# Kernel tuning notes

Hardware: AMD Instinct MI355X
Metric: run time of the kernel (lower is better)

The kernel has to match this reference:

```python
import math
import jax, jax.numpy as jnp
import numpy as np

BS, C, HH, HW = 32, 64, 128, 128   # x is NCHW; C == dim
S0, S1 = 2, 2                      # patch size
DIM = 64
K = 512                            # num_embeddings


def setup_inputs() -> dict:
    key = jax.random.key(0)
    k1, k2 = jax.random.split(key)
    x = jax.random.normal(k1, (BS, C, HH, HW), dtype=jnp.float32)
    embed = jax.random.normal(k2, (S0, S1, DIM, K), dtype=jnp.float32) * 0.02
    return {"x": x, "embed": embed}


def reference(x, embed):
    # eval-mode forward (not training): sample = one_hot(argmax(probs))
    bs, Cc, hH, hW = x.shape
    rH, rW = hH // S0, hW // S1
    xp = jnp.transpose(x, (0, 2, 3, 1))                          # [b, hH, hW, C]
    xb = xp.reshape(bs, rH, S0, rW, S1, Cc)
    xb = jnp.transpose(xb, (0, 1, 3, 2, 4, 5))                   # [b, rH, rW, s0, s1, C]
    flat = xb.reshape(-1, S0 * S1 * Cc)                          # [T, D]
    E = embed.reshape(-1, K)                                     # [D, K]
    # squared-distance via matmul
    distances = (jnp.sum(flat * flat, axis=1, keepdims=True)
                 - 2.0 * (flat @ E)
                 + jnp.sum(E * E, axis=0, keepdims=True))        # [T, K]
    logits = jax.nn.log_softmax(-distances, axis=-1)             # dist.logits (normalized)
    probs = jnp.exp(logits)                                      # dist.probs
    embed_ind_flat = jnp.argmax(probs, axis=-1)                  # [T]
    sample = jax.nn.one_hot(embed_ind_flat, K, dtype=flat.dtype) # [T, K]
    embed_ind = embed_ind_flat.reshape(bs, rH, rW)
    quantize = jnp.einsum('tk,hwdk->thwd', sample, embed)        # [T, s0, s1, dim]
    quantize = quantize.reshape(bs, rH, rW, S0, S1, Cc)
    quantize = jnp.transpose(quantize, (0, 1, 3, 2, 4, 5)).reshape(bs, hH, hW, Cc)
    quantize = jnp.transpose(quantize, (0, 3, 1, 2))             # [b, C, hH, hW]
    KL = jnp.where(probs == 0, 0.0, probs * (logits + math.log(K)))
    diff = KL.sum() / bs * (32 * 32 * 3.0)
    diff = diff * 0.0
    avg_probs = jnp.mean(sample, axis=1)                         # [T] (faithful: mean over K)
    perplexity = jnp.exp(-jnp.sum(avg_probs * jnp.log(avg_probs + 1e-10), axis=-1))
    return quantize, diff, embed_ind, perplexity
```

## Files before the change

### kernel.cpp

```cpp
#include <hip/hip_runtime.h>


#define OFF_DIFF    33554432
#define OFF_IND     33554433
#define OFF_PERP    33685505

typedef __attribute__((ext_vector_type(8))) short short8;
typedef __attribute__((ext_vector_type(4))) float f32x4;

__device__ __forceinline__ unsigned short f2bf(float f) {
    unsigned int u = __float_as_uint(f);
    return (unsigned short)((u + 0x7FFFu + ((u >> 16) & 1u)) >> 16);
}
__device__ __forceinline__ float bf2f(unsigned short h) {
    return __uint_as_float(((unsigned int)h) << 16);
}

__device__ __forceinline__ void gload_lds16(const void* g, void* l) {
    __builtin_amdgcn_global_load_lds(
        (const __attribute__((address_space(1))) unsigned int*)g,
        (__attribute__((address_space(3))) unsigned int*)l, 16, 0, 0);
}

__global__ void vq_split(const float* __restrict__ E,
                         float* __restrict__ Et,
                         short* __restrict__ EhiSw,
                         short* __restrict__ EloSw,
                         float* __restrict__ ssqe,
                         float* __restrict__ out) {
    const int k = blockIdx.x;
    const int t = threadIdx.x;
    float v[4];
    #pragma unroll
    for (int j = 0; j < 4; ++j) v[j] = E[(t * 4 + j) * 512 + k];
    *(float4*)&Et[k * 256 + t * 4] = make_float4(v[0], v[1], v[2], v[3]);

    unsigned short h[4], l[4];
    #pragma unroll
    for (int j = 0; j < 4; ++j) {
        h[j] = f2bf(v[j]);
        l[j] = f2bf(v[j] - bf2f(h[j]));
    }
    uint2 H = make_uint2((unsigned)h[0] | ((unsigned)h[1] << 16),
                         (unsigned)h[2] | ((unsigned)h[3] << 16));
    uint2 L = make_uint2((unsigned)l[0] | ((unsigned)l[1] << 16),
                         (unsigned)l[2] | ((unsigned)l[3] << 16));
    int pos = k * 256 + 8 * ((t >> 1) ^ (k & 7)) + (t & 1) * 4;
    *(uint2*)&EhiSw[pos] = H;
    *(uint2*)&EloSw[pos] = L;

    float s = fmaf(v[0], v[0], fmaf(v[1], v[1], fmaf(v[2], v[2], v[3] * v[3])));
    #pragma unroll
    for (int m = 1; m < 64; m <<= 1) s += __shfl_xor(s, m, 64);
    if (t == 0) {
        ssqe[k] = s;
        if (k == 0) {
            out[OFF_DIFF] = 0.0f;
            out[OFF_PERP] = 0.0f;
        }
    }
}

__device__ __forceinline__ void stage4(short* Th, short* Tl, int lt, int f,
                                       int dbase,
                                       float a, float b, float c, float d) {
    int idx = lt * 256 + (dbase ^ (f << 3));
    unsigned short h0 = f2bf(a), h1 = f2bf(b), h2 = f2bf(c), h3 = f2bf(d);
    *(uint2*)&Th[idx] = make_uint2((unsigned)h0 | ((unsigned)h1 << 16),
                                   (unsigned)h2 | ((unsigned)h3 << 16));
    unsigned short l0 = f2bf(a - bf2f(h0)), l1 = f2bf(b - bf2f(h1));
    unsigned short l2 = f2bf(c - bf2f(h2)), l3 = f2bf(d - bf2f(h3));
    *(uint2*)&Tl[idx] = make_uint2((unsigned)l0 | ((unsigned)l1 << 16),
                                   (unsigned)l2 | ((unsigned)l3 << 16));
}

#define MFMA(A, B, C) __builtin_amdgcn_mfma_f32_16x16x32_bf16(A, B, C, 0, 0, 0)
#define FSWZ(lt) ((((lt) >> 1) ^ ((lt) >> 4)) & 7)

__global__ __launch_bounds__(256, 4)
void vq_main_mfma(const float* __restrict__ x,
                  const float* __restrict__ Et,
                  const short* __restrict__ EhiSw,
                  const short* __restrict__ EloSw,
                  const float* __restrict__ ssqe,
                  float* __restrict__ out) {
    __shared__ __attribute__((aligned(16))) unsigned char smem[35328];
    short* Thi = (short*)smem;
    short* Tlo = (short*)(smem + 16384);
    float* Q   = (float*)smem;
    float* ssqe_sh = (float*)(smem + 33024);
    int*   kstar   = (int*)(smem + 35072);

    const int g   = blockIdx.x;
    const int b   = g >> 6;
    const int rh  = g & 63;
    const int tid = threadIdx.x;
    const int wv  = tid >> 6;
    const int ln  = tid & 63;
    const int r   = ln & 15;
    const int tq  = ln >> 4;
    const int tokr = wv * 16 + r;

    ssqe_sh[tid]       = ssqe[tid];
    ssqe_sh[tid + 256] = ssqe[tid + 256];

    short8 Bh[8], Bl[8];
    const float* xrow = x + (size_t)b * 1048576 + (size_t)rh * 256;

    #pragma unroll
    for (int hp = 0; hp < 2; ++hp) {
        #pragma unroll
        for (int i = 0; i < 2; ++i) {
            int j     = tid + i * 256;
            int col4h = j & 15;
            int rest  = j >> 4;
            int c4    = rest & 15;
            int s0    = rest >> 4;
            const float* p = xrow + (c4 * 4) * 16384 + s0 * 128 + hp * 64 + col4h * 4;
            float4 v0 = *(const float4*)(p);
            float4 v1 = *(const float4*)(p + 16384);
            float4 v2 = *(const float4*)(p + 32768);
            float4 v3 = *(const float4*)(p + 49152);
            int ltA = col4h * 2, ltB = ltA + 1;
            int fA = FSWZ(ltA), fB = FSWZ(ltB);
            int d0 = s0 * 128 + c4 * 4, d1 = d0 + 64;
            stage4(Thi, Tlo, ltA, fA, d0, v0.x, v1.x, v2.x, v3.x);
            stage4(Thi, Tlo, ltA, fA, d1, v0.y, v1.y, v2.y, v3.y);
            stage4(Thi, Tlo, ltB, fB, d0, v0.z, v1.z, v2.z, v3.z);
            stage4(Thi, Tlo, ltB, fB, d1, v0.w, v1.w, v2.w, v3.w);
        }
        __syncthreads();
        if ((tokr >> 5) == hp) {
            int lt = tokr & 31;
            int f  = FSWZ(lt);
            #pragma unroll
            for (int ks = 0; ks < 8; ++ks) {
                int idx = lt * 256 + ((ks * 32 + tq * 8) ^ (f << 3));
                Bh[ks] = *(const short8*)&Thi[idx];
                Bl[ks] = *(const short8*)&Tlo[idx];
            }
        }
        __syncthreads();
    }

    {
        const char* hs = (const char*)EhiSw;
        const char* ls = (const char*)EloSw;
        char* d = (char*)smem;
        int o = wv * 1024 + ln * 16;
        gload_lds16(hs + o,        d + wv * 1024);
        gload_lds16(hs + o + 4096, d + wv * 1024 + 4096);
        gload_lds16(ls + o,        d + wv * 1024 + 8192);
        gload_lds16(ls + o + 4096, d + wv * 1024 + 12288);
    }
    __syncthreads();

    float best  = __builtin_inff();
    int   besti = 0;
    int   cur   = 0;

    for (int ct = 0; ct < 32; ++ct) {
        if (ct < 31) {
            const char* hs = (const char*)EhiSw + (ct + 1) * 8192;
            const char* ls = (const char*)EloSw + (ct + 1) * 8192;
            char* d = (char*)smem + (cur ^ 1) * 16384;
            int o = wv * 1024 + ln * 16;
            gload_lds16(hs + o,        d + wv * 1024);
            gload_lds16(hs + o + 4096, d + wv * 1024 + 4096);
            gload_lds16(ls + o,        d + wv * 1024 + 8192);
            gload_lds16(ls + o + 4096, d + wv * 1024 + 12288);
        }
        const short* bh = (const short*)(smem + cur * 16384);
        const short* bl = bh + 4096;
        f32x4 ae = {0.f, 0.f, 0.f, 0.f};
        f32x4 ao = {0.f, 0.f, 0.f, 0.f};
        #pragma unroll
        for (int ks = 0; ks < 8; ks += 2) {
            int off0 = r * 256 + 8 * ((ks * 4 + tq) ^ (r & 7));
            short8 ah0 = *(const short8*)&bh[off0];
            short8 al0 = *(const short8*)&bl[off0];
            int off1 = r * 256 + 8 * (((ks + 1) * 4 + tq) ^ (r & 7));
            short8 ah1 = *(const short8*)&bh[off1];
            short8 al1 = *(const short8*)&bl[off1];
            ae = MFMA(ah0, Bh[ks], ae);
            ao = MFMA(ah1, Bh[ks + 1], ao);
            ae = MFMA(ah0, Bl[ks], ae);
            ao = MFMA(ah1, Bl[ks + 1], ao);
            ae = MFMA(al0, Bh[ks], ae);
            ao = MFMA(al1, Bh[ks + 1], ao);
        }
        float4 sq = *(const float4*)&ssqe_sh[ct * 16 + tq * 4];
        int kb = ct * 16 + tq * 4;
        float s0v = fmaf(-2.0f, ae[0] + ao[0], sq.x);
        float s1v = fmaf(-2.0f, ae[1] + ao[1], sq.y);
        float s2v = fmaf(-2.0f, ae[2] + ao[2], sq.z);
        float s3v = fmaf(-2.0f, ae[3] + ao[3], sq.w);
        if (s0v < best) { best = s0v; besti = kb;     }
        if (s1v < best) { best = s1v; besti = kb + 1; }
        if (s2v < best) { best = s2v; besti = kb + 2; }
        if (s3v < best) { best = s3v; besti = kb + 3; }
        __syncthreads();
        cur ^= 1;
    }

    #pragma unroll
    for (int m = 16; m <= 32; m <<= 1) {
        float ob = __shfl_xor(best, m, 64);
        int   oi = __shfl_xor(besti, m, 64);
        if (ob < best || (ob == best && oi < besti)) { best = ob; besti = oi; }
    }
    if (tq == 0) {
        kstar[tokr] = besti;
        out[OFF_IND + (size_t)g * 64 + tokr] = (float)besti;
    }
    __syncthreads();

    #pragma unroll
    for (int hp = 0; hp < 2; ++hp) {
        if (hp) __syncthreads();
        {
            int qt = tid & 31, part = tid >> 5;
            const float* Erow = Et + (size_t)kstar[hp * 32 + qt] * 256 + part * 32;
            float* qrow = Q + qt * 257 + part * 32;
            #pragma unroll
            for (int u = 0; u < 8; ++u) {
                float4 vv = *(const float4*)(Erow + u * 4);
                qrow[u * 4]     = vv.x;
                qrow[u * 4 + 1] = vv.y;
                qrow[u * 4 + 2] = vv.z;
                qrow[u * 4 + 3] = vv.w;
            }
        }
        __syncthreads();
        float* ob2 = out + (size_t)b * 1048576 + rh * 256 + hp * 64;
        #pragma unroll
        for (int i = 0; i < 8; ++i) {
            int j     = tid + i * 256;
            int col4h = j & 15;
            int rest  = j >> 4;
            int c  = rest >> 1;
            int s0 = rest & 1;
            int ltA = col4h * 2, ltB = ltA + 1;
            int d0 = s0 * 128 + c, d1 = d0 + 64;
            float4 v;
            v.x = Q[ltA * 257 + d0];
            v.y = Q[ltA * 257 + d1];
            v.z = Q[ltB * 257 + d0];
            v.w = Q[ltB * 257 + d1];
            *(float4*)(ob2 + c * 16384 + s0 * 128 + col4h * 4) = v;
        }
    }
}

__global__ void vq_prep(const float* __restrict__ E,
                        float* __restrict__ ssqe,
                        float* __restrict__ out) {
    int k = blockIdx.x * 256 + threadIdx.x;
    float acc = 0.0f;
    #pragma unroll 8
    for (int d = 0; d < 256; ++d) {
        float e = E[d * 512 + k];
        acc = fmaf(e, e, acc);
    }
    ssqe[k] = acc;
    if (k == 0) { out[OFF_DIFF] = 0.0f; out[OFF_PERP] = 0.0f; }
}

__global__ __launch_bounds__(256, 2)
void vq_main_f32(const float* __restrict__ x,
                 const float* __restrict__ E,
                 const float* __restrict__ ssqe,
                 float* __restrict__ out) {
    __shared__ float A[256 * 64];
    __shared__ float redD[4][64];
    __shared__ int   redI[4][64];
    __shared__ int   kstar_sh[64];

    const int g = blockIdx.x, b = g >> 6, rh = g & 63, tid = threadIdx.x;
    const float* xbase = x + (size_t)b * 1048576 + rh * 256;

    #pragma unroll
    for (int i = 0; i < 16; ++i) {
        int j = tid + i * 256;
        int row = j >> 5, col4 = j & 31;
        int c = row >> 1, s0 = row & 1;
        const float4 v = *(const float4*)(xbase + c * 16384 + s0 * 128 + col4 * 4);
        int tokk = col4 * 2;
        int d0 = s0 * 128 + c, d1 = d0 + 64;
        *(float2*)&A[d0 * 64 + tokk] = make_float2(v.x, v.z);
        *(float2*)&A[d1 * 64 + tokk] = make_float2(v.y, v.w);
    }
    __syncthreads();

    const int wave = tid >> 6, lane = tid & 63;
    float ssq = 0.0f;
    #pragma unroll 8
    for (int d = 0; d < 256; ++d) { float a = A[d * 64 + lane]; ssq = fmaf(a, a, ssq); }

    const int K0 = __builtin_amdgcn_readfirstlane(wave * 128);
    float best = __builtin_inff();
    int besti = 0;
    for (int chunk = 0; chunk < 8; ++chunk) {
        const int k0 = K0 + chunk * 16;
        const float* __restrict__ Ep = E + k0;
        float acc[16];
        #pragma unroll
        for (int j = 0; j < 16; ++j) acc[j] = 0.0f;
        #pragma unroll 4
        for (int d = 0; d < 256; ++d) {
            float a = A[d * 64 + lane];
            #pragma unroll
            for (int j = 0; j < 16; ++j) acc[j] = fmaf(a, Ep[d * 512 + j], acc[j]);
        }
        #pragma unroll
        for (int j = 0; j < 16; ++j) {
            float dist = (ssq - 2.0f * acc[j]) + ssqe[k0 + j];
            if (dist < best) { best = dist; besti = k0 + j; }
        }
    }
    redD[wave][lane] = best; redI[wave][lane] = besti;
    __syncthreads();
    if (tid < 64) {
        float bd = redD[0][tid]; int bi = redI[0][tid];
        #pragma unroll
        for (int w = 1; w < 4; ++w) {
            float dd = redD[w][tid];
            if (dd < bd) { bd = dd; bi = redI[w][tid]; }
        }
        kstar_sh[tid] = bi;
        out[OFF_IND + g * 64 + tid] = (float)bi;
    }
    __syncthreads();
    float* obase = out + (size_t)b * 1048576 + rh * 256;
    #pragma unroll
    for (int i = 0; i < 16; ++i) {
        int j = tid + i * 256;
        int row = j >> 5, col4 = j & 31;
        int c = row >> 1, s0 = row & 1;
        int tokA = col4 * 2, tokB = tokA + 1;
        int kA = kstar_sh[tokA], kB = kstar_sh[tokB];
        int d0 = s0 * 128 + c, d1 = d0 + 64;
        float4 v;
        v.x = E[d0 * 512 + kA]; v.y = E[d1 * 512 + kA];
        v.z = E[d0 * 512 + kB]; v.w = E[d1 * 512 + kB];
        *(float4*)(obase + c * 16384 + s0 * 128 + col4 * 4) = v;
    }
}

extern "C" void kernel_launch(void* const* d_in, const int* in_sizes, int n_in,
                              void* d_out, int out_size, void* d_ws, size_t ws_size,
                              hipStream_t stream) {
    const float* x = (const float*)d_in[0];
    const float* E = (const float*)d_in[1];
    float* out = (float*)d_out;

    float* ssqe  = (float*)d_ws;
    float* Et    = (float*)((char*)d_ws + 4096);
    short* EhiSw = (short*)((char*)d_ws + 528384);
    short* EloSw = (short*)((char*)d_ws + 790528);
    const size_t need = 1052672;

    if (ws_size >= need) {
        hipLaunchKernelGGL(vq_split, dim3(512), dim3(64), 0, stream,
                           E, Et, EhiSw, EloSw, ssqe, out);
        hipLaunchKernelGGL(vq_main_mfma, dim3(2048), dim3(256), 0, stream,
                           x, Et, EhiSw, EloSw, ssqe, out);
    } else {
        hipLaunchKernelGGL(vq_prep, dim3(2), dim3(256), 0, stream, E, ssqe, out);
        hipLaunchKernelGGL(vq_main_f32, dim3(2048), dim3(256), 0, stream,
                           x, E, ssqe, out);
    }
}
```

Measured before the change: 305.1 us.

## Process 128 tokens per block to reuse codebook tiles across two token sets

Each block now handles two row-pairs (128 tokens) instead of 64, so each wave holds two 16-token B fragments and every codebook tile loaded into LDS feeds twice as many MFMAs. The grid is halved and launch bounds drop to 3 blocks per SM to fit the extra B registers and accumulators. This is meant to halve codebook LDS traffic and tile loads per token. The cost is higher register pressure, lower occupancy and fewer blocks.

New measurement: 372.1 us. 1.22x slower.

```diff
diff --git a/kernel.cpp b/kernel.cpp
--- a/kernel.cpp
+++ b/kernel.cpp
@@ -77,14 +77,14 @@
 #define MFMA(A, B, C) __builtin_amdgcn_mfma_f32_16x16x32_bf16(A, B, C, 0, 0, 0)
 #define FSWZ(lt) ((((lt) >> 1) ^ ((lt) >> 4)) & 7)
 
-__global__ __launch_bounds__(256, 4)
+__global__ __launch_bounds__(256, 3)
 void vq_main_mfma(const float* __restrict__ x,
                   const float* __restrict__ Et,
                   const short* __restrict__ EhiSw,
                   const short* __restrict__ EloSw,
                   const float* __restrict__ ssqe,
                   float* __restrict__ out) {
-    __shared__ __attribute__((aligned(16))) unsigned char smem[35328];
+    __shared__ __attribute__((aligned(16))) unsigned char smem[35584];
     short* Thi = (short*)smem;
     short* Tlo = (short*)(smem + 16384);
     float* Q   = (float*)smem;
@@ -92,23 +92,23 @@
     int*   kstar   = (int*)(smem + 35072);
 
     const int g   = blockIdx.x;
-    const int b   = g >> 6;
-    const int rh  = g & 63;
+    const int b   = g >> 5;
+    const int rh2 = g & 31;
     const int tid = threadIdx.x;
     const int wv  = tid >> 6;
     const int ln  = tid & 63;
     const int r   = ln & 15;
     const int tq  = ln >> 4;
-    const int tokr = wv * 16 + r;
 
     ssqe_sh[tid]       = ssqe[tid];
     ssqe_sh[tid + 256] = ssqe[tid + 256];
 
-    short8 Bh[8], Bl[8];
-    const float* xrow = x + (size_t)b * 1048576 + (size_t)rh * 256;
-
-    #pragma unroll
-    for (int hp = 0; hp < 2; ++hp) {
+    short8 Bh0[8], Bl0[8], Bh1[8], Bl1[8];
+
+    #pragma unroll
+    for (int p = 0; p < 4; ++p) {
+        const int rh_p = rh2 * 2 + (p >> 1);
+        const float* xrow = x + (size_t)b * 1048576 + (size_t)rh_p * 256;
         #pragma unroll
         for (int i = 0; i < 2; ++i) {
             int j     = tid + i * 256;
@@ -116,11 +116,12 @@
             int rest  = j >> 4;
             int c4    = rest & 15;
             int s0    = rest >> 4;
-            const float* p = xrow + (c4 * 4) * 16384 + s0 * 128 + hp * 64 + col4h * 4;
-            float4 v0 = *(const float4*)(p);
-            float4 v1 = *(const float4*)(p + 16384);
-            float4 v2 = *(const float4*)(p + 32768);
-            float4 v3 = *(const float4*)(p + 49152);
+            const float* pp = xrow + (c4 * 4) * 16384 + s0 * 128
+                              + (p & 1) * 64 + col4h * 4;
+            float4 v0 = *(const float4*)(pp);
+            float4 v1 = *(const float4*)(pp + 16384);
+            float4 v2 = *(const float4*)(pp + 32768);
+            float4 v3 = *(const float4*)(pp + 49152);
             int ltA = col4h * 2, ltB = ltA + 1;
             int fA = FSWZ(ltA), fB = FSWZ(ltB);
             int d0 = s0 * 128 + c4 * 4, d1 = d0 + 64;
@@ -130,14 +131,16 @@
             stage4(Thi, Tlo, ltB, fB, d1, v0.w, v1.w, v2.w, v3.w);
         }
         __syncthreads();
-        if ((tokr >> 5) == hp) {
-            int lt = tokr & 31;
-            int f  = FSWZ(lt);
+        if (wv == p) {
+            int f0 = FSWZ(r), f1 = FSWZ(16 + r);
             #pragma unroll
             for (int ks = 0; ks < 8; ++ks) {
-                int idx = lt * 256 + ((ks * 32 + tq * 8) ^ (f << 3));
-                Bh[ks] = *(const short8*)&Thi[idx];
-                Bl[ks] = *(const short8*)&Tlo[idx];
+                int i0 = r * 256 + ((ks * 32 + tq * 8) ^ (f0 << 3));
+                Bh0[ks] = *(const short8*)&Thi[i0];
+                Bl0[ks] = *(const short8*)&Tlo[i0];
+                int i1 = (16 + r) * 256 + ((ks * 32 + tq * 8) ^ (f1 << 3));
+                Bh1[ks] = *(const short8*)&Thi[i1];
+                Bl1[ks] = *(const short8*)&Tlo[i1];
             }
         }
         __syncthreads();
@@ -155,9 +158,9 @@
     }
     __syncthreads();
 
-    float best  = __builtin_inff();
-    int   besti = 0;
-    int   cur   = 0;
+    float best0 = __builtin_inff(), best1 = __builtin_inff();
+    int   bi0 = 0, bi1 = 0;
+    int   cur = 0;
 
     for (int ct = 0; ct < 32; ++ct) {
         if (ct < 31) {
@@ -172,8 +175,8 @@
         }
         const short* bh = (const short*)(smem + cur * 16384);
         const short* bl = bh + 4096;
-        f32x4 ae = {0.f, 0.f, 0.f, 0.f};
-        f32x4 ao = {0.f, 0.f, 0.f, 0.f};
+        f32x4 a0e = {0.f,0.f,0.f,0.f}, a0o = {0.f,0.f,0.f,0.f};
+        f32x4 a1e = {0.f,0.f,0.f,0.f}, a1o = {0.f,0.f,0.f,0.f};
         #pragma unroll
         for (int ks = 0; ks < 8; ks += 2) {
             int off0 = r * 256 + 8 * ((ks * 4 + tq) ^ (r & 7));
@@ -182,45 +185,58 @@
             int off1 = r * 256 + 8 * (((ks + 1) * 4 + tq) ^ (r & 7));
             short8 ah1 = *(const short8*)&bh[off1];
             short8 al1 = *(const short8*)&bl[off1];
-            ae = MFMA(ah0, Bh[ks], ae);
-            ao = MFMA(ah1, Bh[ks + 1], ao);
-            ae = MFMA(ah0, Bl[ks], ae);
-            ao = MFMA(ah1, Bl[ks + 1], ao);
-            ae = MFMA(al0, Bh[ks], ae);
-            ao = MFMA(al1, Bh[ks + 1], ao);
+            a0e = MFMA(ah0, Bh0[ks],     a0e);
+            a1e = MFMA(ah0, Bh1[ks],     a1e);
+            a0o = MFMA(ah1, Bh0[ks + 1], a0o);
+            a1o = MFMA(ah1, Bh1[ks + 1], a1o);
+            a0e = MFMA(ah0, Bl0[ks],     a0e);
+            a1e = MFMA(ah0, Bl1[ks],     a1e);
+            a0o = MFMA(ah1, Bl0[ks + 1], a0o);
+            a1o = MFMA(ah1, Bl1[ks + 1], a1o);
+            a0e = MFMA(al0, Bh0[ks],     a0e);
+            a1e = MFMA(al0, Bh1[ks],     a1e);
+            a0o = MFMA(al1, Bh0[ks + 1], a0o);
+            a1o = MFMA(al1, Bh1[ks + 1], a1o);
         }
         float4 sq = *(const float4*)&ssqe_sh[ct * 16 + tq * 4];
         int kb = ct * 16 + tq * 4;
-        float s0v = fmaf(-2.0f, ae[0] + ao[0], sq.x);
-        float s1v = fmaf(-2.0f, ae[1] + ao[1], sq.y);
-        float s2v = fmaf(-2.0f, ae[2] + ao[2], sq.z);
-        float s3v = fmaf(-2.0f, ae[3] + ao[3], sq.w);
-        if (s0v < best) { best = s0v; besti = kb;     }
-        if (s1v < best) { best = s1v; besti = kb + 1; }
-        if (s2v < best) { best = s2v; besti = kb + 2; }
-        if (s3v < best) { best = s3v; besti = kb + 3; }
+        #pragma unroll
+        for (int jj = 0; jj < 4; ++jj) {
+            float sqj = (jj == 0) ? sq.x : (jj == 1) ? sq.y : (jj == 2) ? sq.z : sq.w;
+            float s0v = fmaf(-2.0f, a0e[jj] + a0o[jj], sqj);
+            float s1v = fmaf(-2.0f, a1e[jj] + a1o[jj], sqj);
+            if (s0v < best0) { best0 = s0v; bi0 = kb + jj; }
+            if (s1v < best1) { best1 = s1v; bi1 = kb + jj; }
+        }
         __syncthreads();
         cur ^= 1;
     }
 
     #pragma unroll
     for (int m = 16; m <= 32; m <<= 1) {
-        float ob = __shfl_xor(best, m, 64);
-        int   oi = __shfl_xor(besti, m, 64);
-        if (ob < best || (ob == best && oi < besti)) { best = ob; besti = oi; }
+        float ob = __shfl_xor(best0, m, 64);
+        int   oi = __shfl_xor(bi0, m, 64);
+        if (ob < best0 || (ob == best0 && oi < bi0)) { best0 = ob; bi0 = oi; }
+        float pb = __shfl_xor(best1, m, 64);
+        int   pi = __shfl_xor(bi1, m, 64);
+        if (pb < best1 || (pb == best1 && pi < bi1)) { best1 = pb; bi1 = pi; }
     }
     if (tq == 0) {
-        kstar[tokr] = besti;
-        out[OFF_IND + (size_t)g * 64 + tokr] = (float)besti;
-    }
-    __syncthreads();
-
-    #pragma unroll
-    for (int hp = 0; hp < 2; ++hp) {
-        if (hp) __syncthreads();
+        int t0 = wv * 32 + r, t1 = t0 + 16;
+        kstar[t0] = bi0;
+        kstar[t1] = bi1;
+        size_t ib = (size_t)OFF_IND + (size_t)b * 4096 + (size_t)rh2 * 128;
+        out[ib + t0] = (float)bi0;
+        out[ib + t1] = (float)bi1;
+    }
+    __syncthreads();
+
+    #pragma unroll
+    for (int p = 0; p < 4; ++p) {
+        if (p) __syncthreads();
         {
             int qt = tid & 31, part = tid >> 5;
-            const float* Erow = Et + (size_t)kstar[hp * 32 + qt] * 256 + part * 32;
+            const float* Erow = Et + (size_t)kstar[p * 32 + qt] * 256 + part * 32;
             float* qrow = Q + qt * 257 + part * 32;
             #pragma unroll
             for (int u = 0; u < 8; ++u) {
@@ -232,7 +248,8 @@
             }
         }
         __syncthreads();
-        float* ob2 = out + (size_t)b * 1048576 + rh * 256 + hp * 64;
+        const int rh_p = rh2 * 2 + (p >> 1);
+        float* ob2 = out + (size_t)b * 1048576 + (size_t)rh_p * 256 + (p & 1) * 64;
         #pragma unroll
         for (int i = 0; i < 8; ++i) {
             int j     = tid + i * 256;
@@ -363,7 +380,7 @@
     if (ws_size >= need) {
         hipLaunchKernelGGL(vq_split, dim3(512), dim3(64), 0, stream,
                            E, Et, EhiSw, EloSw, ssqe, out);
-        hipLaunchKernelGGL(vq_main_mfma, dim3(2048), dim3(256), 0, stream,
+        hipLaunchKernelGGL(vq_main_mfma, dim3(1024), dim3(256), 0, stream,
                            x, Et, EhiSw, EloSw, ssqe, out);
     } else {
         hipLaunchKernelGGL(vq_prep, dim3(2), dim3(256), 0, stream, E, ssqe, out);
```
